# Kernel tuning notes

Measured on AMD Instinct MI355X. Metric: run time of the kernel, lower is better.

## Reference

```python
import jax, jax.numpy as jnp
import numpy as np

SIGMA = 1.0          # args.sigma
THRESH = 0.35        # hard-coded stop threshold in gat_selection_feature
MAX_ITERS = 48       # bound on the data-dependent greedy loop (gain saturates to 0)


def setup_inputs() -> dict:
    key = jax.random.key(0)
    k1, k2, k3, k4 = jax.random.split(key, 4)
    B, N, F = 8192, 64, 32  # dst nodes, neighbors per node, feature size (attn_weights is 32x1)
    return {
        "mail": jax.random.normal(k1, (B, N, F), jnp.float32),
        "attn_w": jax.random.normal(k2, (F, 1), jnp.float32),
        "src_norm": jax.random.uniform(k3, (B, N), jnp.float32, minval=0.5, maxval=1.0),
        "dst_norm": jax.random.uniform(k4, (B,), jnp.float32, minval=0.5, maxval=1.0),
    }


def _pairwise_dist(x):
    # torch.cdist: Euclidean pairwise distances, [B,N,F] -> [B,N,N]
    sq = jnp.sum(x * x, axis=-1)
    d2 = sq[:, :, None] + sq[:, None, :] - 2.0 * jnp.einsum('bnf,bmf->bnm', x, x)
    return jnp.sqrt(jnp.maximum(d2, 0.0))


def reference(mail, attn_w, src_norm, dst_norm):
    # source-degree normalization (degs^-0.5 applied to feat_src before update_all)
    feat = mail * src_norm[..., None]                     # [B,N,F]
    B, N, Fd = feat.shape

    dists = _pairwise_dist(feat)                          # [B,N,N]
    mean_d = dists.mean(axis=(-2, -1))[:, None, None]     # per-batch scalar mean
    sims = jnp.exp(-dists / (SIGMA * mean_d))             # [B,N,N]

    # attention_weights(features): constant across greedy iterations
    logits = jnp.einsum('bnf,fo->bn', feat, attn_w)       # [B,N]
    attention = jax.nn.softmax(logits, axis=1)            # [B,N]

    bidx = jnp.arange(B)

    def step(carry, _):
        cache, acc, active = carry                        # cache [B,N], acc [B,F], active scalar bool
        gain = jnp.sum(jnp.maximum(sims, cache[:, None, :]) - cache[:, None, :], axis=-1)
        gain = gain * attention                           # [B,N]
        max_value = gain.max()
        sel = jnp.argmax(gain, axis=1)                    # [B]
        w = jnp.where(active, jnp.float32(1.0), jnp.float32(0.0))
        acc = acc + w * feat[bidx, sel]                   # append-then-check: terminating iter included
        cache = jnp.where(active, jnp.maximum(sims[bidx, sel], cache), cache)
        active = jnp.logical_and(active, max_value >= THRESH)
        return (cache, acc, active), None

    cache0 = jnp.zeros((B, N), feat.dtype)
    acc0 = jnp.zeros((B, Fd), feat.dtype)
    (_, acc, _), _ = jax.lax.scan(step, (cache0, acc0, jnp.array(True)), None, length=MAX_ITERS)

    # destination in-degree normalization
    return acc * dst_norm[:, None]
```

## Files before the change

kernel.cpp:

```cpp
#include <hip/hip_runtime.h>

#define B_TOT 8192
#define NN 64
#define FF 32
#define ITERS 48
#define THRESH 0.35f

#define TSTOP_OFF (458752)
#define ATTN_OFF  (524288)
#define SIMS_OFF  (4194304)
#define WS_NEEDED (SIMS_OFF + (size_t)B_TOT * NN * NN * 4)

__global__ __launch_bounds__(64) void gat_greedy_kernel(
    const float* __restrict__ mail,
    const float* __restrict__ attn_w,
    const float* __restrict__ src_norm,
    int* __restrict__ tmax_ws,
    unsigned char* __restrict__ sels_ws)
{
    const int b = blockIdx.x;
    const int lane = threadIdx.x;

    __shared__ __align__(16) float sims[NN * 65];
    __shared__ __align__(16) float c_lds[NN];
    __shared__ float qarr[NN];
    __shared__ float sarr[NN];

    const float* __restrict__ myrow = mail + ((size_t)b * NN + lane) * FF;
    float a[FF];
#pragma unroll
    for (int k = 0; k < 8; ++k) {
        const float4 v = reinterpret_cast<const float4*>(myrow)[k];
        a[4*k+0] = v.x; a[4*k+1] = v.y; a[4*k+2] = v.z; a[4*k+3] = v.w;
    }
    const float sn = src_norm[b * NN + lane];

    float q0 = 0.f, q1 = 0.f, q2 = 0.f, q3 = 0.f;
#pragma unroll
    for (int k = 0; k < 8; ++k) {
        q0 = fmaf(a[4*k+0], a[4*k+0], q0);
        q1 = fmaf(a[4*k+1], a[4*k+1], q1);
        q2 = fmaf(a[4*k+2], a[4*k+2], q2);
        q3 = fmaf(a[4*k+3], a[4*k+3], q3);
    }
    const float q = (q0 + q1) + (q2 + q3);

    float lg = 0.f;
#pragma unroll
    for (int f = 0; f < FF; ++f) lg = fmaf(a[f], attn_w[f], lg);
    lg *= sn;

    qarr[lane] = q;
    sarr[lane] = sn;
    __syncthreads();

    float mx = lg;
#pragma unroll
    for (int off = 32; off > 0; off >>= 1)
        mx = fmaxf(mx, __shfl_xor(mx, off, 64));
    const float ex = __expf(lg - mx);
    float se = ex;
#pragma unroll
    for (int off = 32; off > 0; off >>= 1)
        se += __shfl_xor(se, off, 64);
    const float attn = ex / se;

    const float sqn = sn * sn * q;
    float dsum = 0.f;
    for (int m = 0; m < NN; ++m) {
        const float4* __restrict__ Am =
            reinterpret_cast<const float4*>(mail + ((size_t)b * NN + m) * FF);
        float g0 = 0.f, g1 = 0.f, g2 = 0.f, g3 = 0.f;
#pragma unroll
        for (int k = 0; k < 8; ++k) {
            const float4 v = Am[k];
            g0 = fmaf(a[4*k+0], v.x, g0);
            g1 = fmaf(a[4*k+1], v.y, g1);
            g2 = fmaf(a[4*k+2], v.z, g2);
            g3 = fmaf(a[4*k+3], v.w, g3);
        }
        const float g  = (g0 + g1) + (g2 + g3);
        const float sm = sarr[m];
        const float qm = qarr[m];
        const float sqm = sm * sm * qm;
        const float d2  = (sqn - 2.f * (sn * sm) * g) + sqm;
        const float d   = sqrtf(fmaxf(d2, 0.f));
        dsum += d;
        sims[lane * 65 + m] = d;
    }

    float tot = dsum;
#pragma unroll
    for (int off = 32; off > 0; off >>= 1)
        tot += __shfl_xor(tot, off, 64);
    const float meand = tot * (1.f / (float)(NN * NN));
    const float inv   = -1.f / meand;

    float srow[NN];
#pragma unroll
    for (int m = 0; m < NN; ++m) {
        const float d = sims[lane * 65 + m];
        const float s = __expf(d * inv);
        srow[m] = s;
        sims[lane * 65 + m] = s;
    }
#pragma unroll
    for (int m = 0; m < NN; ++m)
        asm volatile("" : "+v"(srow[m]));

    c_lds[lane] = 0.f;
    float c_reg = 0.f;
    __syncthreads();

    int firstBelow = ITERS;
    bool seenBelow = false;

    for (int t = 0; t < ITERS; ++t) {
        float gain = 0.f;
#pragma unroll
        for (int k = 0; k < 16; ++k) {
            const float4 cv = reinterpret_cast<const float4*>(c_lds)[k];
            gain += fmaxf(srow[4*k+0] - cv.x, 0.f);
            gain += fmaxf(srow[4*k+1] - cv.y, 0.f);
            gain += fmaxf(srow[4*k+2] - cv.z, 0.f);
            gain += fmaxf(srow[4*k+3] - cv.w, 0.f);
        }
        gain *= attn;

        float gv = gain; int gi = lane;
#pragma unroll
        for (int off = 32; off > 0; off >>= 1) {
            const float ov = __shfl_xor(gv, off, 64);
            const int   oi = __shfl_xor(gi, off, 64);
            if (ov > gv || (ov == gv && oi < gi)) { gv = ov; gi = oi; }
        }

        if (!seenBelow && gv < THRESH) { firstBelow = t; seenBelow = true; }
        if (lane == 0) sels_ws[(size_t)b * ITERS + t] = (unsigned char)gi;

        const float srl = sims[gi * 65 + lane];
        c_reg = fmaxf(c_reg, srl);
        c_lds[lane] = c_reg;
        __syncthreads();
    }

    if (lane == 0) atomicMax(tmax_ws, firstBelow);
}

__global__ __launch_bounds__(64) void gat_fusedA_kernel(
    const float* __restrict__ mail,
    const float* __restrict__ attn_w,
    const float* __restrict__ src_norm,
    int* __restrict__ tmax_ws,
    int* __restrict__ tstop_ws,
    unsigned char* __restrict__ sels_ws,
    float* __restrict__ sims_g,
    float* __restrict__ attn_g)
{
    const int b = blockIdx.x;
    const int lane = threadIdx.x;

    __shared__ __align__(16) float sims[NN * 65];
    __shared__ __align__(16) float c_lds[NN];
    __shared__ float qarr[NN];
    __shared__ float sarr[NN];

    const float* __restrict__ myrow = mail + ((size_t)b * NN + lane) * FF;
    float a[FF];
#pragma unroll
    for (int k = 0; k < 8; ++k) {
        const float4 v = reinterpret_cast<const float4*>(myrow)[k];
        a[4*k+0] = v.x; a[4*k+1] = v.y; a[4*k+2] = v.z; a[4*k+3] = v.w;
    }
    const float sn = src_norm[b * NN + lane];

    float q0 = 0.f, q1 = 0.f, q2 = 0.f, q3 = 0.f;
#pragma unroll
    for (int k = 0; k < 8; ++k) {
        q0 = fmaf(a[4*k+0], a[4*k+0], q0);
        q1 = fmaf(a[4*k+1], a[4*k+1], q1);
        q2 = fmaf(a[4*k+2], a[4*k+2], q2);
        q3 = fmaf(a[4*k+3], a[4*k+3], q3);
    }
    const float q = (q0 + q1) + (q2 + q3);

    float lg = 0.f;
#pragma unroll
    for (int f = 0; f < FF; ++f) lg = fmaf(a[f], attn_w[f], lg);
    lg *= sn;

    qarr[lane] = q;
    sarr[lane] = sn;
    __syncthreads();

    float mx = lg;
#pragma unroll
    for (int off = 32; off > 0; off >>= 1)
        mx = fmaxf(mx, __shfl_xor(mx, off, 64));
    const float ex = __expf(lg - mx);
    float se = ex;
#pragma unroll
    for (int off = 32; off > 0; off >>= 1)
        se += __shfl_xor(se, off, 64);
    const float attn = ex / se;

    const float sqn = sn * sn * q;
    float dsum = 0.f;
    for (int m = 0; m < NN; ++m) {
        const float4* __restrict__ Am =
            reinterpret_cast<const float4*>(mail + ((size_t)b * NN + m) * FF);
        float g0 = 0.f, g1 = 0.f, g2 = 0.f, g3 = 0.f;
#pragma unroll
        for (int k = 0; k < 8; ++k) {
            const float4 v = Am[k];
            g0 = fmaf(a[4*k+0], v.x, g0);
            g1 = fmaf(a[4*k+1], v.y, g1);
            g2 = fmaf(a[4*k+2], v.z, g2);
            g3 = fmaf(a[4*k+3], v.w, g3);
        }
        const float g  = (g0 + g1) + (g2 + g3);
        const float sm = sarr[m];
        const float qm = qarr[m];
        const float sqm = sm * sm * qm;
        const float d2  = (sqn - 2.f * (sn * sm) * g) + sqm;
        const float d   = sqrtf(fmaxf(d2, 0.f));
        dsum += d;
        sims[lane * 65 + m] = d;
    }

    float tot = dsum;
#pragma unroll
    for (int off = 32; off > 0; off >>= 1)
        tot += __shfl_xor(tot, off, 64);
    const float meand = tot * (1.f / (float)(NN * NN));
    const float inv   = -1.f / meand;

    float srow[NN];
#pragma unroll
    for (int m = 0; m < NN; ++m) {
        const float d = sims[lane * 65 + m];
        const float s = __expf(d * inv);
        srow[m] = s;
        sims[lane * 65 + m] = s;
    }
#pragma unroll
    for (int m = 0; m < NN; ++m)
        asm volatile("" : "+v"(srow[m]));

    c_lds[lane] = 0.f;
    float c_reg = 0.f;
    __syncthreads();

    int firstBelow = ITERS;

    for (int t = 0; t < ITERS; ++t) {
        float gain = 0.f;
#pragma unroll
        for (int k = 0; k < 16; ++k) {
            const float4 cv = reinterpret_cast<const float4*>(c_lds)[k];
            gain += fmaxf(srow[4*k+0] - cv.x, 0.f);
            gain += fmaxf(srow[4*k+1] - cv.y, 0.f);
            gain += fmaxf(srow[4*k+2] - cv.z, 0.f);
            gain += fmaxf(srow[4*k+3] - cv.w, 0.f);
        }
        gain *= attn;

        float gv = gain; int gi = lane;
#pragma unroll
        for (int off = 32; off > 0; off >>= 1) {
            const float ov = __shfl_xor(gv, off, 64);
            const int   oi = __shfl_xor(gi, off, 64);
            if (ov > gv || (ov == gv && oi < gi)) { gv = ov; gi = oi; }
        }

        if (lane == 0) sels_ws[(size_t)b * ITERS + t] = (unsigned char)gi;

        const float srl = sims[gi * 65 + lane];
        c_reg = fmaxf(c_reg, srl);
        c_lds[lane] = c_reg;
        __syncthreads();

        if (gv < THRESH) { firstBelow = t; break; }
    }

    if (lane == 0) {
        atomicMax(tmax_ws, firstBelow);
        tstop_ws[b] = firstBelow;
    }

    if (firstBelow < ITERS - 1) {
        attn_g[b * NN + lane] = attn;
        float* __restrict__ simsb = sims_g + (size_t)b * NN * NN;
        for (int m = 0; m < NN; ++m)
            simsb[m * NN + lane] = sims[m * 65 + lane];
    }
}

__global__ __launch_bounds__(64) void gat_greedyB_kernel(
    const float* __restrict__ sims_g,
    const float* __restrict__ attn_g,
    const int* __restrict__ tmax_ws,
    const int* __restrict__ tstop_ws,
    unsigned char* __restrict__ sels_ws)
{
    const int b = blockIdx.x;
    const int lane = threadIdx.x;

    const int fb   = tstop_ws[b];
    const int tEnd = min(ITERS - 1, *tmax_ws);
    if (fb >= tEnd) return;

    __shared__ __align__(16) float c_lds[NN];

    const float* __restrict__ simsb = sims_g + (size_t)b * NN * NN;

    float srow[NN];
    const float4* __restrict__ rp =
        reinterpret_cast<const float4*>(simsb + (size_t)lane * NN);
#pragma unroll
    for (int k = 0; k < 16; ++k) {
        const float4 v = rp[k];
        srow[4*k+0] = v.x; srow[4*k+1] = v.y;
        srow[4*k+2] = v.z; srow[4*k+3] = v.w;
    }
#pragma unroll
    for (int m = 0; m < NN; ++m)
        asm volatile("" : "+v"(srow[m]));

    const float attn = attn_g[b * NN + lane];

    float c_reg = 0.f;
    const unsigned char* __restrict__ sb = sels_ws + (size_t)b * ITERS;
    for (int j = 0; j <= fb; ++j) {
        const int sel = sb[j];
        c_reg = fmaxf(c_reg, simsb[sel * NN + lane]);
    }
    c_lds[lane] = c_reg;
    __syncthreads();

    for (int t = fb + 1; t <= tEnd; ++t) {
        float gain = 0.f;
#pragma unroll
        for (int k = 0; k < 16; ++k) {
            const float4 cv = reinterpret_cast<const float4*>(c_lds)[k];
            gain += fmaxf(srow[4*k+0] - cv.x, 0.f);
            gain += fmaxf(srow[4*k+1] - cv.y, 0.f);
            gain += fmaxf(srow[4*k+2] - cv.z, 0.f);
            gain += fmaxf(srow[4*k+3] - cv.w, 0.f);
        }
        gain *= attn;

        float gv = gain; int gi = lane;
#pragma unroll
        for (int off = 32; off > 0; off >>= 1) {
            const float ov = __shfl_xor(gv, off, 64);
            const int   oi = __shfl_xor(gi, off, 64);
            if (ov > gv || (ov == gv && oi < gi)) { gv = ov; gi = oi; }
        }

        if (lane == 0) sels_ws[(size_t)b * ITERS + t] = (unsigned char)gi;

        const float srl = simsb[gi * NN + lane];
        c_reg = fmaxf(c_reg, srl);
        c_lds[lane] = c_reg;
        __syncthreads();
    }
}

__global__ __launch_bounds__(64) void gat_accum_kernel(
    const float* __restrict__ mail,
    const float* __restrict__ src_norm,
    const float* __restrict__ dst_norm,
    const int* __restrict__ tmax_ws,
    const unsigned char* __restrict__ sels_ws,
    float* __restrict__ out)
{
    const int lane = threadIdx.x & 31;
    const int b = blockIdx.x * 2 + (threadIdx.x >> 5);
    const int C = min(ITERS, *tmax_ws + 1);
    const unsigned char* __restrict__ sb = sels_ws + (size_t)b * ITERS;
    float acc = 0.f;
    for (int t = 0; t < C; ++t) {
        const int sel = sb[t];
        acc = fmaf(mail[((size_t)b * NN + sel) * FF + lane],
                   src_norm[b * NN + sel], acc);
    }
    out[b * FF + lane] = acc * dst_norm[b];
}

extern "C" void kernel_launch(void* const* d_in, const int* in_sizes, int n_in,
                              void* d_out, int out_size, void* d_ws, size_t ws_size,
                              hipStream_t stream)
{
    const float* mail     = (const float*)d_in[0];
    const float* attn_w   = (const float*)d_in[1];
    const float* src_norm = (const float*)d_in[2];
    const float* dst_norm = (const float*)d_in[3];
    float* out = (float*)d_out;

    int* tmax_ws = (int*)d_ws;
    unsigned char* sels_ws = (unsigned char*)d_ws + 16;

    hipMemsetAsync(d_ws, 0, 4, stream);

    if (ws_size >= WS_NEEDED) {
        int*   tstop_ws = (int*)((char*)d_ws + TSTOP_OFF);
        float* attn_g   = (float*)((char*)d_ws + ATTN_OFF);
        float* sims_g   = (float*)((char*)d_ws + SIMS_OFF);
        gat_fusedA_kernel<<<dim3(B_TOT), dim3(64), 0, stream>>>(
            mail, attn_w, src_norm, tmax_ws, tstop_ws, sels_ws, sims_g, attn_g);
        gat_greedyB_kernel<<<dim3(B_TOT), dim3(64), 0, stream>>>(
            sims_g, attn_g, tmax_ws, tstop_ws, sels_ws);
    } else {
        gat_greedy_kernel<<<dim3(B_TOT), dim3(64), 0, stream>>>(
            mail, attn_w, src_norm, tmax_ws, sels_ws);
    }
    gat_accum_kernel<<<dim3(B_TOT / 2), dim3(64), 0, stream>>>(
        mail, src_norm, dst_norm, tmax_ws, sels_ws, out);
}
```

Baseline: 252.9 us.

## Fuse greedy continuation with accumulation and write sims unconditionally before loop

Merges the second greedy phase and the final feature accumulation into one kernel: selections made past each batch's own stop point are kept in LDS, and the first 32 lanes then accumulate the selected features and write the output. This removes one kernel launch and the global round trip of those selections. The sims and attention spills from the first kernel now happen unconditionally before its greedy loop, not only when the batch stops early. That adds 16KB of global writes per batch even when phase B never reads them, in exchange for issuing the stores earlier where they may overlap with the loop.

Result: faster. 237.8 us (-6.0%).

```diff
diff --git a/kernel.cpp b/kernel.cpp
--- a/kernel.cpp
+++ b/kernel.cpp
@@ -251,6 +251,13 @@
     float c_reg = 0.f;
     __syncthreads();
 
+    attn_g[b * NN + lane] = attn;
+    {
+        float* __restrict__ simsb = sims_g + (size_t)b * NN * NN;
+        for (int m = 0; m < NN; ++m)
+            simsb[m * NN + lane] = sims[m * 65 + lane];
+    }
+
     int firstBelow = ITERS;
 
     for (int t = 0; t < ITERS; ++t) {
@@ -287,83 +294,95 @@
         atomicMax(tmax_ws, firstBelow);
         tstop_ws[b] = firstBelow;
     }
-
-    if (firstBelow < ITERS - 1) {
-        attn_g[b * NN + lane] = attn;
-        float* __restrict__ simsb = sims_g + (size_t)b * NN * NN;
-        for (int m = 0; m < NN; ++m)
-            simsb[m * NN + lane] = sims[m * 65 + lane];
-    }
 }
 
-__global__ __launch_bounds__(64) void gat_greedyB_kernel(
+__global__ __launch_bounds__(64) void gat_greedyB_acc_kernel(
     const float* __restrict__ sims_g,
     const float* __restrict__ attn_g,
+    const float* __restrict__ mail,
+    const float* __restrict__ src_norm,
+    const float* __restrict__ dst_norm,
     const int* __restrict__ tmax_ws,
     const int* __restrict__ tstop_ws,
-    unsigned char* __restrict__ sels_ws)
+    const unsigned char* __restrict__ sels_ws,
+    float* __restrict__ out)
 {
     const int b = blockIdx.x;
     const int lane = threadIdx.x;
 
     const int fb   = tstop_ws[b];
-    const int tEnd = min(ITERS - 1, *tmax_ws);
-    if (fb >= tEnd) return;
+    const int Tmax = *tmax_ws;
+    const int tEnd = min(ITERS - 1, Tmax);
 
     __shared__ __align__(16) float c_lds[NN];
-
-    const float* __restrict__ simsb = sims_g + (size_t)b * NN * NN;
-
-    float srow[NN];
-    const float4* __restrict__ rp =
-        reinterpret_cast<const float4*>(simsb + (size_t)lane * NN);
-#pragma unroll
-    for (int k = 0; k < 16; ++k) {
-        const float4 v = rp[k];
-        srow[4*k+0] = v.x; srow[4*k+1] = v.y;
-        srow[4*k+2] = v.z; srow[4*k+3] = v.w;
-    }
-#pragma unroll
-    for (int m = 0; m < NN; ++m)
-        asm volatile("" : "+v"(srow[m]));
-
-    const float attn = attn_g[b * NN + lane];
-
-    float c_reg = 0.f;
+    __shared__ int sel_lds[ITERS];
+
     const unsigned char* __restrict__ sb = sels_ws + (size_t)b * ITERS;
-    for (int j = 0; j <= fb; ++j) {
-        const int sel = sb[j];
-        c_reg = fmaxf(c_reg, simsb[sel * NN + lane]);
-    }
-    c_lds[lane] = c_reg;
-    __syncthreads();
-
-    for (int t = fb + 1; t <= tEnd; ++t) {
-        float gain = 0.f;
+
+    if (fb < tEnd) {
+        const float* __restrict__ simsb = sims_g + (size_t)b * NN * NN;
+
+        float srow[NN];
+        const float4* __restrict__ rp =
+            reinterpret_cast<const float4*>(simsb + (size_t)lane * NN);
 #pragma unroll
         for (int k = 0; k < 16; ++k) {
-            const float4 cv = reinterpret_cast<const float4*>(c_lds)[k];
-            gain += fmaxf(srow[4*k+0] - cv.x, 0.f);
-            gain += fmaxf(srow[4*k+1] - cv.y, 0.f);
-            gain += fmaxf(srow[4*k+2] - cv.z, 0.f);
-            gain += fmaxf(srow[4*k+3] - cv.w, 0.f);
-        }
-        gain *= attn;
-
-        float gv = gain; int gi = lane;
-#pragma unroll
-        for (int off = 32; off > 0; off >>= 1) {
-            const float ov = __shfl_xor(gv, off, 64);
-            const int   oi = __shfl_xor(gi, off, 64);
-            if (ov > gv || (ov == gv && oi < gi)) { gv = ov; gi = oi; }
-        }
-
-        if (lane == 0) sels_ws[(size_t)b * ITERS + t] = (unsigned char)gi;
-
-        const float srl = simsb[gi * NN + lane];
-        c_reg = fmaxf(c_reg, srl);
+            const float4 v = rp[k];
+            srow[4*k+0] = v.x; srow[4*k+1] = v.y;
+            srow[4*k+2] = v.z; srow[4*k+3] = v.w;
+        }
+#pragma unroll
+        for (int m = 0; m < NN; ++m)
+            asm volatile("" : "+v"(srow[m]));
+
+        const float attn = attn_g[b * NN + lane];
+
+        float c_reg = 0.f;
+        for (int j = 0; j <= fb; ++j) {
+            const int sel = sb[j];
+            c_reg = fmaxf(c_reg, simsb[sel * NN + lane]);
+        }
         c_lds[lane] = c_reg;
         __syncthreads();
+
+        for (int t = fb + 1; t <= tEnd; ++t) {
+            float gain = 0.f;
+#pragma unroll
+            for (int k = 0; k < 16; ++k) {
+                const float4 cv = reinterpret_cast<const float4*>(c_lds)[k];
+                gain += fmaxf(srow[4*k+0] - cv.x, 0.f);
+                gain += fmaxf(srow[4*k+1] - cv.y, 0.f);
+                gain += fmaxf(srow[4*k+2] - cv.z, 0.f);
+                gain += fmaxf(srow[4*k+3] - cv.w, 0.f);
+            }
+            gain *= attn;
+
+            float gv = gain; int gi = lane;
+#pragma unroll
+            for (int off = 32; off > 0; off >>= 1) {
+                const float ov = __shfl_xor(gv, off, 64);
+                const int   oi = __shfl_xor(gi, off, 64);
+                if (ov > gv || (ov == gv && oi < gi)) { gv = ov; gi = oi; }
+            }
+
+            if (lane == 0) sel_lds[t] = gi;
+
+            const float srl = simsb[gi * NN + lane];
+            c_reg = fmaxf(c_reg, srl);
+            c_lds[lane] = c_reg;
+            __syncthreads();
+        }
+    }
+
+    if (lane < FF) {
+        const int C = min(ITERS, Tmax + 1);
+        float acc = 0.f;
+        for (int t = 0; t < C; ++t) {
+            const int sel = (t <= fb) ? (int)sb[t] : sel_lds[t];
+            acc = fmaf(mail[((size_t)b * NN + sel) * FF + lane],
+                       src_norm[b * NN + sel], acc);
+        }
+        out[b * FF + lane] = acc * dst_norm[b];
     }
 }
 
@@ -409,12 +428,13 @@
         float* sims_g   = (float*)((char*)d_ws + SIMS_OFF);
         gat_fusedA_kernel<<<dim3(B_TOT), dim3(64), 0, stream>>>(
             mail, attn_w, src_norm, tmax_ws, tstop_ws, sels_ws, sims_g, attn_g);
-        gat_greedyB_kernel<<<dim3(B_TOT), dim3(64), 0, stream>>>(
-            sims_g, attn_g, tmax_ws, tstop_ws, sels_ws);
+        gat_greedyB_acc_kernel<<<dim3(B_TOT), dim3(64), 0, stream>>>(
+            sims_g, attn_g, mail, src_norm, dst_norm,
+            tmax_ws, tstop_ws, sels_ws, out);
     } else {
         gat_greedy_kernel<<<dim3(B_TOT), dim3(64), 0, stream>>>(
             mail, attn_w, src_norm, tmax_ws, sels_ws);
-    }
-    gat_accum_kernel<<<dim3(B_TOT / 2), dim3(64), 0, stream>>>(
-        mail, src_norm, dst_norm, tmax_ws, sels_ws, out);
+        gat_accum_kernel<<<dim3(B_TOT / 2), dim3(64), 0, stream>>>(
+            mail, src_norm, dst_norm, tmax_ws, sels_ws, out);
+    }
 }
```
